# Kernel tuning notes

Measured on AMD Instinct MI355X. Metric: run time of the kernel, lower is better.

## Reference

```python
import jax, jax.numpy as jnp
import numpy as np

N_NODES = 100000
HID = 128
N_EDGES = 600000


def sage_conv(h, src, dst, Wl, bl, Wr, n_nodes):
    # PyG SAGEConv (mean aggr): out = lin_l(mean_{j->i} h_j) + lin_r(h_i)
    msgs = h[src]                                               # [E, d] gather
    agg = jax.ops.segment_sum(msgs, dst, num_segments=n_nodes)  # [N, d]
    cnt = jax.ops.segment_sum(jnp.ones((src.shape[0], 1), h.dtype), dst,
                              num_segments=n_nodes)             # [N, 1]
    mean = agg / jnp.maximum(cnt, 1.0)                          # isolated nodes -> 0
    return mean @ Wl.T + bl + h @ Wr.T


def setup_inputs() -> dict:
    key = jax.random.key(0)
    ks = jax.random.split(key, 8)
    scale = 1.0 / np.sqrt(HID)
    x = jnp.arange(N_NODES, dtype=jnp.int64) if jax.config.jax_enable_x64 else jnp.arange(N_NODES, dtype=jnp.int32)
    edge_index = jax.random.randint(ks[0], (2, N_EDGES), 0, N_NODES)
    emb = jax.random.normal(ks[1], (N_NODES, HID), dtype=jnp.float32) * scale
    Wl1 = jax.random.normal(ks[2], (HID, HID), dtype=jnp.float32) * scale
    bl1 = jnp.zeros((HID,), jnp.float32)
    Wr1 = jax.random.normal(ks[3], (HID, HID), dtype=jnp.float32) * scale
    Wl2 = jax.random.normal(ks[4], (HID, HID), dtype=jnp.float32) * scale
    bl2 = jnp.zeros((HID,), jnp.float32)
    Wr2 = jax.random.normal(ks[5], (HID, HID), dtype=jnp.float32) * scale
    return {"x": x, "edge_index": edge_index, "emb": emb,
            "Wl1": Wl1, "bl1": bl1, "Wr1": Wr1,
            "Wl2": Wl2, "bl2": bl2, "Wr2": Wr2}


def reference(x, edge_index, emb, Wl1, bl1, Wr1, Wl2, bl2, Wr2):
    src, dst = edge_index[0], edge_index[1]
    n = emb.shape[0]
    h = emb[x]                                          # embedding lookup [N, d]
    h = jax.nn.relu(sage_conv(h, src, dst, Wl1, bl1, Wr1, n))  # dropout = eval identity
    h = jax.nn.relu(sage_conv(h, src, dst, Wl2, bl2, Wr2, n))
    return h
```

## Files before the change

### kernel.cpp

```cpp
#include <hip/hip_runtime.h>

#define HID 128

typedef unsigned short ushort_t;
typedef unsigned int uint_t;
typedef float f32x4 __attribute__((ext_vector_type(4)));
typedef short s16x8 __attribute__((ext_vector_type(8)));

__device__ __forceinline__ ushort_t f2bf(float f) {
  uint_t u = __float_as_uint(f);
  uint_t r = (u + 0x7FFFu + ((u >> 16) & 1u)) >> 16;
  return (ushort_t)r;
}
__device__ __forceinline__ float bfLo(uint_t v) { return __uint_as_float(v << 16); }
__device__ __forceinline__ float bfHi(uint_t v) { return __uint_as_float(v & 0xFFFF0000u); }

__device__ __forceinline__ uint4 pack8(const float4& lo, const float4& hi) {
  uint4 p;
  p.x = (uint_t)f2bf(lo.x) | ((uint_t)f2bf(lo.y) << 16);
  p.y = (uint_t)f2bf(lo.z) | ((uint_t)f2bf(lo.w) << 16);
  p.z = (uint_t)f2bf(hi.x) | ((uint_t)f2bf(hi.y) << 16);
  p.w = (uint_t)f2bf(hi.z) | ((uint_t)f2bf(hi.w) << 16);
  return p;
}

__global__ __launch_bounds__(256) void prep_kernel(
    const float* __restrict__ emb, const int* __restrict__ x,
    ushort_t* __restrict__ hb, int N,
    const float* __restrict__ Wl1, const float* __restrict__ Wr1,
    const float* __restrict__ Wl2, const float* __restrict__ Wr2,
    ushort_t* __restrict__ wsw,
    const int* __restrict__ dst, int* __restrict__ deg, int E) {
  int tid = blockIdx.x * 256 + threadIdx.x;
  const int qN = (N + 3) >> 2;
  int gthreads = qN * 16;
  if (tid < gthreads) {
    int r0 = tid >> 4, j = (tid & 15) * 8;
    int r1 = r0 + qN, r2 = r0 + 2 * qN, r3 = r0 + 3 * qN;
    int s0 = x[r0];
    int s1 = (r1 < N) ? x[r1] : s0;
    int s2 = (r2 < N) ? x[r2] : s0;
    int s3 = (r3 < N) ? x[r3] : s0;
    const float* p0 = &emb[(size_t)s0 * HID + j];
    const float* p1 = &emb[(size_t)s1 * HID + j];
    const float* p2 = &emb[(size_t)s2 * HID + j];
    const float* p3 = &emb[(size_t)s3 * HID + j];
    float4 a0 = *(const float4*)p0, a1 = *(const float4*)(p0 + 4);
    float4 b0 = *(const float4*)p1, b1 = *(const float4*)(p1 + 4);
    float4 c0 = *(const float4*)p2, c1 = *(const float4*)(p2 + 4);
    float4 d0 = *(const float4*)p3, d1 = *(const float4*)(p3 + 4);
    *(uint4*)&hb[(size_t)r0 * HID + j] = pack8(a0, a1);
    if (r1 < N) *(uint4*)&hb[(size_t)r1 * HID + j] = pack8(b0, b1);
    if (r2 < N) *(uint4*)&hb[(size_t)r2 * HID + j] = pack8(c0, c1);
    if (r3 < N) *(uint4*)&hb[(size_t)r3 * HID + j] = pack8(d0, d1);
    return;
  }
  tid -= gthreads;
  if (tid < 65536) {
    const float* srcs[4] = {Wl1, Wr1, Wl2, Wr2};
    int m = tid >> 14, idx = tid & 16383;
    int j = idx & 7;
    int lane = (idx >> 3) & 63;
    int nt = (idx >> 9) & 7;
    int ks = (idx >> 12) & 3;
    int row = nt * 16 + (lane & 15);
    int col = ks * 32 + (lane >> 4) * 8 + j;
    wsw[tid] = f2bf(srcs[m][row * HID + col]);
    return;
  }
  tid -= 65536;
  if (tid < E) atomicAdd(&deg[dst[tid]], 1);
}

__global__ __launch_bounds__(256) void scan1_kernel(
    const int* __restrict__ deg, int* __restrict__ offsets,
    int* __restrict__ sums, int N) {
  __shared__ int s[256];
  int b = blockIdx.x, t = threadIdx.x;
  int base = b * 1024 + t * 4;
  int v0 = 0, v1 = 0, v2 = 0, v3 = 0;
  if (base + 0 < N) v0 = deg[base + 0];
  if (base + 1 < N) v1 = deg[base + 1];
  if (base + 2 < N) v2 = deg[base + 2];
  if (base + 3 < N) v3 = deg[base + 3];
  int mySum = v0 + v1 + v2 + v3;
  s[t] = mySum;
  __syncthreads();
  for (int off = 1; off < 256; off <<= 1) {
    int v = (t >= off) ? s[t - off] : 0;
    __syncthreads();
    s[t] += v;
    __syncthreads();
  }
  int excl = s[t] - mySum;
  if (t == 255) sums[b] = s[255];
  if (base + 0 < N) offsets[base + 0] = excl;
  if (base + 1 < N) offsets[base + 1] = excl + v0;
  if (base + 2 < N) offsets[base + 2] = excl + v0 + v1;
  if (base + 3 < N) offsets[base + 3] = excl + v0 + v1 + v2;
}

__global__ __launch_bounds__(256) void scan3_kernel(
    int* __restrict__ offsets, const int* __restrict__ sums,
    int* __restrict__ cursor, int N, int E, int nb) {
  __shared__ int red[256];
  int t = threadIdx.x;
  int chunk = (blockIdx.x * 256) >> 10;
  red[t] = (t < chunk) ? sums[t] : 0;
  __syncthreads();
  for (int off = 128; off > 0; off >>= 1) {
    if (t < off) red[t] += red[t + off];
    __syncthreads();
  }
  int prefix = red[0];
  int i = blockIdx.x * 256 + t;
  if (i < N) {
    int v = offsets[i] + prefix;
    offsets[i] = v;
    cursor[i] = v;
  } else if (i == N) {
    offsets[N] = E;
  }
}

__global__ __launch_bounds__(256) void fill_kernel(
    const int* __restrict__ src, const int* __restrict__ dst,
    int* __restrict__ cursor, int* __restrict__ csr, int E) {
  int e = blockIdx.x * 256 + threadIdx.x;
  if (e >= E) return;
  int d = dst[e];
  int pos = atomicAdd(&cursor[d], 1);
  csr[pos] = src[e];
}

__global__ __launch_bounds__(256) void aggregate_kernel(
    const ushort_t* __restrict__ hb, const int* __restrict__ offsets,
    const int* __restrict__ csr, ushort_t* __restrict__ meanb, int N) {
  int t = threadIdx.x;
  int node = blockIdx.x * 16 + (t >> 4);
  if (node >= N) return;
  int l15 = t & 15;
  int o0 = offsets[node], o1 = offsets[node + 1];
  int last = o1 - 1;

  float acc[8];
#pragma unroll
  for (int i = 0; i < 8; i++) acc[i] = 0.f;

  for (int e = o0; e < o1; e += 8) {
    uint4 v[8];
    float m[8];
#pragma unroll
    for (int i = 0; i < 8; i++) {
      int idx = e + i;
      bool val = idx < o1;
      int s = csr[val ? idx : last];
      v[i] = *(const uint4*)&hb[(size_t)s * HID + l15 * 8];
      m[i] = val ? 1.f : 0.f;
    }
#pragma unroll
    for (int i = 0; i < 8; i++) {
      acc[0] = fmaf(m[i], bfLo(v[i].x), acc[0]);
      acc[1] = fmaf(m[i], bfHi(v[i].x), acc[1]);
      acc[2] = fmaf(m[i], bfLo(v[i].y), acc[2]);
      acc[3] = fmaf(m[i], bfHi(v[i].y), acc[3]);
      acc[4] = fmaf(m[i], bfLo(v[i].z), acc[4]);
      acc[5] = fmaf(m[i], bfHi(v[i].z), acc[5]);
      acc[6] = fmaf(m[i], bfLo(v[i].w), acc[6]);
      acc[7] = fmaf(m[i], bfHi(v[i].w), acc[7]);
    }
  }

  int d = o1 - o0;
  float inv = 1.0f / (float)(d > 1 ? d : 1);
  uint4 p;
  p.x = (uint_t)f2bf(acc[0] * inv) | ((uint_t)f2bf(acc[1] * inv) << 16);
  p.y = (uint_t)f2bf(acc[2] * inv) | ((uint_t)f2bf(acc[3] * inv) << 16);
  p.z = (uint_t)f2bf(acc[4] * inv) | ((uint_t)f2bf(acc[5] * inv) << 16);
  p.w = (uint_t)f2bf(acc[6] * inv) | ((uint_t)f2bf(acc[7] * inv) << 16);
  *(uint4*)&meanb[(size_t)node * HID + l15 * 8] = p;
}

__global__ __launch_bounds__(256) void mfma_gemm_kernel(
    const ushort_t* __restrict__ meanb, const ushort_t* __restrict__ hb,
    const ushort_t* __restrict__ WlS, const ushort_t* __restrict__ WrS,
    const float* __restrict__ bias, float* __restrict__ outF,
    ushort_t* __restrict__ outB, int N, int outIsBf16) {
  __shared__ ushort_t ws[32768];
  const int t = threadIdx.x;
  const int wave = t >> 6;
  const int lane = t & 63;
  const int rowBase = (blockIdx.x * 4 + wave) * 32;
  const int l15 = lane & 15;
  const int quad = lane >> 4;
  const int kq = quad * 8;
  const bool active = rowBase < N;

  int r0 = rowBase + l15;       if (r0 >= N) r0 = N - 1;
  int r1 = rowBase + 16 + l15;  if (r1 >= N) r1 = N - 1;

  s16x8 a[2][2][4];
  if (active) {
#pragma unroll
    for (int ks = 0; ks < 4; ks++) {
      a[0][0][ks] = *(const s16x8*)&meanb[(size_t)r0 * HID + ks * 32 + kq];
      a[0][1][ks] = *(const s16x8*)&meanb[(size_t)r1 * HID + ks * 32 + kq];
      a[1][0][ks] = *(const s16x8*)&hb[(size_t)r0 * HID + ks * 32 + kq];
      a[1][1][ks] = *(const s16x8*)&hb[(size_t)r1 * HID + ks * 32 + kq];
    }
  }

#pragma unroll
  for (int it = 0; it < 8; it++) {
    int o = (it * 256 + t) * 8;
    *(s16x8*)&ws[o] = *(const s16x8*)&WlS[o];
    *(s16x8*)&ws[16384 + o] = *(const s16x8*)&WrS[o];
  }
  __syncthreads();

  if (active) {
    f32x4 acc[2][8];
#pragma unroll
    for (int mt = 0; mt < 2; mt++)
#pragma unroll
      for (int nt = 0; nt < 8; nt++) acc[mt][nt] = (f32x4){0.f, 0.f, 0.f, 0.f};

#pragma unroll
    for (int half = 0; half < 2; half++) {
      const int hbase = half * 16384;
#pragma unroll
      for (int ks = 0; ks < 4; ks++)
#pragma unroll
        for (int nt = 0; nt < 8; nt++) {
          s16x8 b = *(const s16x8*)&ws[hbase + ((ks * 8 + nt) * 64 + lane) * 8];
          acc[0][nt] = __builtin_amdgcn_mfma_f32_16x16x32_bf16(a[half][0][ks], b, acc[0][nt], 0, 0, 0);
          acc[1][nt] = __builtin_amdgcn_mfma_f32_16x16x32_bf16(a[half][1][ks], b, acc[1][nt], 0, 0, 0);
        }
    }

#pragma unroll
    for (int mt = 0; mt < 2; mt++) {
#pragma unroll
      for (int nt = 0; nt < 8; nt++) {
        int col = nt * 16 + l15;
        float bv = bias[col];
#pragma unroll
        for (int r = 0; r < 4; r++) {
          int row = rowBase + mt * 16 + quad * 4 + r;
          if (row < N) {
            float v = fmaxf(acc[mt][nt][r] + bv, 0.f);
            if (outIsBf16) outB[(size_t)row * HID + col] = f2bf(v);
            else           outF[(size_t)row * HID + col] = v;
          }
        }
      }
    }
  }
}

extern "C" void kernel_launch(void* const* d_in, const int* in_sizes, int n_in,
                              void* d_out, int out_size, void* d_ws, size_t ws_size,
                              hipStream_t stream) {
  const int* x = (const int*)d_in[0];
  const int* ei = (const int*)d_in[1];
  const float* emb = (const float*)d_in[2];
  const float* Wl1 = (const float*)d_in[3];
  const float* bl1 = (const float*)d_in[4];
  const float* Wr1 = (const float*)d_in[5];
  const float* Wl2 = (const float*)d_in[6];
  const float* bl2 = (const float*)d_in[7];
  const float* Wr2 = (const float*)d_in[8];
  float* out = (float*)d_out;

  const int N = in_sizes[0];
  const int E = in_sizes[1] / 2;
  const int* srcI = ei;
  const int* dstI = ei + E;

  char* p = (char*)d_ws;
  ushort_t* hb = (ushort_t*)p;    p += (size_t)N * HID * sizeof(ushort_t);
  ushort_t* hb2 = (ushort_t*)p;   p += (size_t)N * HID * sizeof(ushort_t);
  ushort_t* meanb = (ushort_t*)p; p += (size_t)N * HID * sizeof(ushort_t);
  ushort_t* wb = (ushort_t*)p;    p += (size_t)4 * 16384 * sizeof(ushort_t);
  int* deg = (int*)p;             p += (size_t)((N + 3) & ~3) * sizeof(int);
  int* offsets = (int*)p;         p += (size_t)((N + 4) & ~3) * sizeof(int);
  int* cursor = (int*)p;          p += (size_t)((N + 3) & ~3) * sizeof(int);
  int* csr = (int*)p;             p += (size_t)((E + 3) & ~3) * sizeof(int);
  int* sums = (int*)p;            p += 256 * sizeof(int);

  ushort_t* Wlb1 = wb;
  ushort_t* Wrb1 = wb + 16384;
  ushort_t* Wlb2 = wb + 32768;
  ushort_t* Wrb2 = wb + 49152;

  const int nScanBlocks = (N + 1023) / 1024;
  const int eBlocks = (E + 255) / 256;
  const int gemmBlocks = (N + 127) / 128;
  const int aggBlocks = (N + 15) / 16;
  const int qN = (N + 3) / 4;
  const int prepBlocks = (qN * 16 + 65536 + E + 255) / 256;

  hipMemsetAsync(deg, 0, (size_t)N * sizeof(int), stream);
  prep_kernel<<<prepBlocks, 256, 0, stream>>>(emb, x, hb, N,
                                              Wl1, Wr1, Wl2, Wr2, wb,
                                              dstI, deg, E);
  scan1_kernel<<<nScanBlocks, 256, 0, stream>>>(deg, offsets, sums, N);
  scan3_kernel<<<(N + 256) / 256, 256, 0, stream>>>(offsets, sums, cursor,
                                                    N, E, nScanBlocks);
  fill_kernel<<<eBlocks, 256, 0, stream>>>(srcI, dstI, cursor, csr, E);

  aggregate_kernel<<<aggBlocks, 256, 0, stream>>>(hb, offsets, csr, meanb, N);
  mfma_gemm_kernel<<<gemmBlocks, 256, 0, stream>>>(meanb, hb, Wlb1, Wrb1, bl1,
                                                   nullptr, hb2, N, 1);

  aggregate_kernel<<<aggBlocks, 256, 0, stream>>>(hb2, offsets, csr, meanb, N);
  mfma_gemm_kernel<<<gemmBlocks, 256, 0, stream>>>(meanb, hb2, Wlb2, Wrb2, bl2,
                                                   out, nullptr, N, 0);
}
```

Measured before the change: 286.6 us.

## Fuse CSR build and input prep into one cooperative persistent kernel

Merges the memset, prep, two scan kernels and the CSR fill into a single cooperative kernel with 1024 persistent blocks, separated by grid-wide syncs. The goal is to remove several kernel launches and the gaps between them in the graph-building front end. The cost is grid.sync overhead and grid-stride loops over fewer threads. The scan now uses 256-element chunks with a per-block serial prefix over block sums, which assumes N/256 stays at or below 512 chunks and fits in 1024 blocks.

```diff
diff --git a/kernel.cpp b/kernel.cpp
--- a/kernel.cpp
+++ b/kernel.cpp
@@ -1,6 +1,10 @@
 #include <hip/hip_runtime.h>
+#include <hip/hip_cooperative_groups.h>
+
+namespace cg = cooperative_groups;
 
 #define HID 128
+#define COOP_BLOCKS 1024
 
 typedef unsigned short ushort_t;
 typedef unsigned int uint_t;
@@ -24,18 +28,41 @@
   return p;
 }
 
-__global__ __launch_bounds__(256) void prep_kernel(
+__global__ __launch_bounds__(256) void front_kernel(
     const float* __restrict__ emb, const int* __restrict__ x,
     ushort_t* __restrict__ hb, int N,
     const float* __restrict__ Wl1, const float* __restrict__ Wr1,
     const float* __restrict__ Wl2, const float* __restrict__ Wr2,
     ushort_t* __restrict__ wsw,
-    const int* __restrict__ dst, int* __restrict__ deg, int E) {
-  int tid = blockIdx.x * 256 + threadIdx.x;
+    const int* __restrict__ srcI, const int* __restrict__ dstI, int E,
+    int* __restrict__ deg, int* __restrict__ offsets,
+    int* __restrict__ cursor, int* __restrict__ csr,
+    int* __restrict__ blockSums) {
+  cg::grid_group grid = cg::this_grid();
+  __shared__ int s[256];
+  const int t = threadIdx.x;
+  const int b = blockIdx.x;
+  const int gtid = b * 256 + t;
+  const int gstride = COOP_BLOCKS * 256;
+
+  for (int i = gtid; i < N; i += gstride)
+    __hip_atomic_store(&deg[i], 0, __ATOMIC_RELAXED, __HIP_MEMORY_SCOPE_AGENT);
+
+  for (int i = gtid; i < 65536; i += gstride) {
+    const float* srcs[4] = {Wl1, Wr1, Wl2, Wr2};
+    int m = i >> 14, idx = i & 16383;
+    int j = idx & 7;
+    int lane = (idx >> 3) & 63;
+    int nt = (idx >> 9) & 7;
+    int ks = (idx >> 12) & 3;
+    int row = nt * 16 + (lane & 15);
+    int col = ks * 32 + (lane >> 4) * 8 + j;
+    wsw[i] = f2bf(srcs[m][row * HID + col]);
+  }
+
   const int qN = (N + 3) >> 2;
-  int gthreads = qN * 16;
-  if (tid < gthreads) {
-    int r0 = tid >> 4, j = (tid & 15) * 8;
+  for (int task = gtid; task < qN * 16; task += gstride) {
+    int r0 = task >> 4, j = (task & 15) * 8;
     int r1 = r0 + qN, r2 = r0 + 2 * qN, r3 = r0 + 3 * qN;
     int s0 = x[r0];
     int s1 = (r1 < N) ? x[r1] : s0;
@@ -53,84 +80,63 @@
     if (r1 < N) *(uint4*)&hb[(size_t)r1 * HID + j] = pack8(b0, b1);
     if (r2 < N) *(uint4*)&hb[(size_t)r2 * HID + j] = pack8(c0, c1);
     if (r3 < N) *(uint4*)&hb[(size_t)r3 * HID + j] = pack8(d0, d1);
-    return;
-  }
-  tid -= gthreads;
-  if (tid < 65536) {
-    const float* srcs[4] = {Wl1, Wr1, Wl2, Wr2};
-    int m = tid >> 14, idx = tid & 16383;
-    int j = idx & 7;
-    int lane = (idx >> 3) & 63;
-    int nt = (idx >> 9) & 7;
-    int ks = (idx >> 12) & 3;
-    int row = nt * 16 + (lane & 15);
-    int col = ks * 32 + (lane >> 4) * 8 + j;
-    wsw[tid] = f2bf(srcs[m][row * HID + col]);
-    return;
-  }
-  tid -= 65536;
-  if (tid < E) atomicAdd(&deg[dst[tid]], 1);
-}
-
-__global__ __launch_bounds__(256) void scan1_kernel(
-    const int* __restrict__ deg, int* __restrict__ offsets,
-    int* __restrict__ sums, int N) {
-  __shared__ int s[256];
-  int b = blockIdx.x, t = threadIdx.x;
-  int base = b * 1024 + t * 4;
-  int v0 = 0, v1 = 0, v2 = 0, v3 = 0;
-  if (base + 0 < N) v0 = deg[base + 0];
-  if (base + 1 < N) v1 = deg[base + 1];
-  if (base + 2 < N) v2 = deg[base + 2];
-  if (base + 3 < N) v3 = deg[base + 3];
-  int mySum = v0 + v1 + v2 + v3;
-  s[t] = mySum;
-  __syncthreads();
-  for (int off = 1; off < 256; off <<= 1) {
-    int v = (t >= off) ? s[t - off] : 0;
+  }
+  grid.sync();
+
+  for (int e = gtid; e < E; e += gstride) atomicAdd(&deg[dstI[e]], 1);
+  grid.sync();
+
+  const int nChunks = (N + 255) >> 8;
+  int myExcl = 0;
+  if (b < nChunks) {
+    int idx = b * 256 + t;
+    int val = (idx < N)
+        ? __hip_atomic_load(&deg[idx], __ATOMIC_RELAXED, __HIP_MEMORY_SCOPE_AGENT)
+        : 0;
+    s[t] = val;
     __syncthreads();
-    s[t] += v;
+    for (int off = 1; off < 256; off <<= 1) {
+      int v = (t >= off) ? s[t - off] : 0;
+      __syncthreads();
+      s[t] += v;
+      __syncthreads();
+    }
+    myExcl = s[t] - val;
+    if (t == 255)
+      __hip_atomic_store(&blockSums[b], s[255], __ATOMIC_RELAXED,
+                         __HIP_MEMORY_SCOPE_AGENT);
+  }
+  grid.sync();
+
+  if (b < nChunks) {
+    int part = 0;
+    for (int i = t; i < b; i += 256)
+      part += __hip_atomic_load(&blockSums[i], __ATOMIC_RELAXED,
+                                __HIP_MEMORY_SCOPE_AGENT);
     __syncthreads();
-  }
-  int excl = s[t] - mySum;
-  if (t == 255) sums[b] = s[255];
-  if (base + 0 < N) offsets[base + 0] = excl;
-  if (base + 1 < N) offsets[base + 1] = excl + v0;
-  if (base + 2 < N) offsets[base + 2] = excl + v0 + v1;
-  if (base + 3 < N) offsets[base + 3] = excl + v0 + v1 + v2;
-}
-
-__global__ __launch_bounds__(256) void scan3_kernel(
-    int* __restrict__ offsets, const int* __restrict__ sums,
-    int* __restrict__ cursor, int N, int E, int nb) {
-  __shared__ int red[256];
-  int t = threadIdx.x;
-  int chunk = (blockIdx.x * 256) >> 10;
-  red[t] = (t < chunk) ? sums[t] : 0;
-  __syncthreads();
-  for (int off = 128; off > 0; off >>= 1) {
-    if (t < off) red[t] += red[t + off];
+    s[t] = part;
     __syncthreads();
-  }
-  int prefix = red[0];
-  int i = blockIdx.x * 256 + t;
-  if (i < N) {
-    int v = offsets[i] + prefix;
-    offsets[i] = v;
-    cursor[i] = v;
-  } else if (i == N) {
-    offsets[N] = E;
-  }
-}
-
-__global__ __launch_bounds__(256) void fill_kernel(
-    const int* __restrict__ src, const int* __restrict__ dst,
-    int* __restrict__ cursor, int* __restrict__ csr, int E) {
-  int e = blockIdx.x * 256 + threadIdx.x;
-  if (e >= E) return;
-  int d = dst[e];
-  int pos = atomicAdd(&cursor[d], 1);
-  csr[pos] = src[e];
+    for (int off = 128; off > 0; off >>= 1) {
+      if (t < off) s[t] += s[t + off];
+      __syncthreads();
+    }
+    int prefix = s[0];
+    int idx = b * 256 + t;
+    if (idx < N) {
+      int v = prefix + myExcl;
+      offsets[idx] = v;
+      __hip_atomic_store(&cursor[idx], v, __ATOMIC_RELAXED,
+                         __HIP_MEMORY_SCOPE_AGENT);
+    }
+    if (b == 0 && t == 0) offsets[N] = E;
+  }
+  grid.sync();
+
+  for (int e = gtid; e < E; e += gstride) {
+    int d = dstI[e];
+    int pos = atomicAdd(&cursor[d], 1);
+    csr[pos] = srcI[e];
+  }
 }
 
 __global__ __launch_bounds__(256) void aggregate_kernel(
@@ -154,8 +160,8 @@
     for (int i = 0; i < 8; i++) {
       int idx = e + i;
       bool val = idx < o1;
-      int s = csr[val ? idx : last];
-      v[i] = *(const uint4*)&hb[(size_t)s * HID + l15 * 8];
+      int sidx = csr[val ? idx : last];
+      v[i] = *(const uint4*)&hb[(size_t)sidx * HID + l15 * 8];
       m[i] = val ? 1.f : 0.f;
     }
 #pragma unroll
@@ -232,9 +238,9 @@
       for (int ks = 0; ks < 4; ks++)
 #pragma unroll
         for (int nt = 0; nt < 8; nt++) {
-          s16x8 b = *(const s16x8*)&ws[hbase + ((ks * 8 + nt) * 64 + lane) * 8];
-          acc[0][nt] = __builtin_amdgcn_mfma_f32_16x16x32_bf16(a[half][0][ks], b, acc[0][nt], 0, 0, 0);
-          acc[1][nt] = __builtin_amdgcn_mfma_f32_16x16x32_bf16(a[half][1][ks], b, acc[1][nt], 0, 0, 0);
+          s16x8 bfrag = *(const s16x8*)&ws[hbase + ((ks * 8 + nt) * 64 + lane) * 8];
+          acc[0][nt] = __builtin_amdgcn_mfma_f32_16x16x32_bf16(a[half][0][ks], bfrag, acc[0][nt], 0, 0, 0);
+          acc[1][nt] = __builtin_amdgcn_mfma_f32_16x16x32_bf16(a[half][1][ks], bfrag, acc[1][nt], 0, 0, 0);
         }
     }
 
@@ -286,28 +292,31 @@
   int* offsets = (int*)p;         p += (size_t)((N + 4) & ~3) * sizeof(int);
   int* cursor = (int*)p;          p += (size_t)((N + 3) & ~3) * sizeof(int);
   int* csr = (int*)p;             p += (size_t)((E + 3) & ~3) * sizeof(int);
-  int* sums = (int*)p;            p += 256 * sizeof(int);
+  int* blockSums = (int*)p;       p += 512 * sizeof(int);
 
   ushort_t* Wlb1 = wb;
   ushort_t* Wrb1 = wb + 16384;
   ushort_t* Wlb2 = wb + 32768;
   ushort_t* Wrb2 = wb + 49152;
 
-  const int nScanBlocks = (N + 1023) / 1024;
-  const int eBlocks = (E + 255) / 256;
   const int gemmBlocks = (N + 127) / 128;
   const int aggBlocks = (N + 15) / 16;
-  const int qN = (N + 3) / 4;
-  const int prepBlocks = (qN * 16 + 65536 + E + 255) / 256;
-
-  hipMemsetAsync(deg, 0, (size_t)N * sizeof(int), stream);
-  prep_kernel<<<prepBlocks, 256, 0, stream>>>(emb, x, hb, N,
-                                              Wl1, Wr1, Wl2, Wr2, wb,
-                                              dstI, deg, E);
-  scan1_kernel<<<nScanBlocks, 256, 0, stream>>>(deg, offsets, sums, N);
-  scan3_kernel<<<(N + 256) / 256, 256, 0, stream>>>(offsets, sums, cursor,
-                                                    N, E, nScanBlocks);
-  fill_kernel<<<eBlocks, 256, 0, stream>>>(srcI, dstI, cursor, csr, E);
+
+  {
+    const float* a_emb = emb; const int* a_x = x;
+    ushort_t* a_hb = hb; int a_N = N;
+    const float* a_Wl1 = Wl1; const float* a_Wr1 = Wr1;
+    const float* a_Wl2 = Wl2; const float* a_Wr2 = Wr2;
+    ushort_t* a_wsw = wb;
+    const int* a_src = srcI; const int* a_dst = dstI; int a_E = E;
+    int* a_deg = deg; int* a_off = offsets; int* a_cur = cursor;
+    int* a_csr = csr; int* a_bs = blockSums;
+    void* args[] = {&a_emb, &a_x, &a_hb, &a_N, &a_Wl1, &a_Wr1, &a_Wl2, &a_Wr2,
+                    &a_wsw, &a_src, &a_dst, &a_E, &a_deg, &a_off, &a_cur,
+                    &a_csr, &a_bs};
+    hipLaunchCooperativeKernel((void*)front_kernel, dim3(COOP_BLOCKS),
+                               dim3(256), args, 0, stream);
+  }
 
   aggregate_kernel<<<aggBlocks, 256, 0, stream>>>(hb, offsets, csr, meanb, N);
   mfma_gemm_kernel<<<gemmBlocks, 256, 0, stream>>>(meanb, hb, Wlb1, Wrb1, bl1,
```

Measured after the change: 745.7 us. 160% more time.
